# Optimization experiments

Hardware: AMD Instinct MI355X
Metric: run time of the kernel (lower is better)

Reference implementation:

```python
import jax, jax.numpy as jnp
import numpy as np

# ---- social-force / MPDM constants (param object in the original) ----
N = 4096           # number of agents (row 0 = robot)
DT = 0.4           # integration timestep [s]
PED_SPEED = 1.0    # desired pedestrian speed [m/s]
K_ATTR = 2.0       # attractive-force gain k
ALPHA = 10.0       # repulsive-force amplitude
PED_RADIUS = 0.3   # pedestrian radius [m]
PED_MASS = 60.0    # pedestrian mass [kg]
BETTA = 0.71       # repulsion range constant
A_COST = 5.0       # deviation (blame) weight a
B_COST = 2.0       # proximity-blame weight b
E_COST = 1.0       # blame length scale e
EPS = 1e-8


def calc_forces(state, goal):
    pos, vel = state[:, :2], state[:, 2:4]
    # attractive force toward goal: k * (v_desired - v_current)
    to_goal = goal - pos
    dist_g = jnp.sqrt(jnp.sum(to_goal * to_goal, axis=1, keepdims=True) + EPS)
    af = K_ATTR * (PED_SPEED * to_goal / dist_g - vel)
    # pairwise repulsive social force, [N,N,2] interaction tensor
    delta = pos[:, None, :] - pos[None, :, :]                 # [N,N,2]
    dist = jnp.sqrt(jnp.sum(delta * delta, axis=-1) + EPS)    # [N,N]
    mag = ALPHA * jnp.exp((2.0 * PED_RADIUS - dist) / BETTA)  # [N,N]
    mag = mag * (1.0 - jnp.eye(pos.shape[0], dtype=pos.dtype))  # no self-force
    rf = jnp.einsum('ij,ijc->ic', mag / dist, delta) / PED_MASS
    return rf, af


def pose_propagation(F, state):
    pos, vel = state[:, :2], state[:, 2:4]
    new_pos = pos + vel * DT + 0.5 * F * (DT * DT)
    new_vel = vel + F * DT
    spd = jnp.sqrt(jnp.sum(new_vel * new_vel, axis=1, keepdims=True) + EPS)
    new_vel = new_vel * jnp.minimum(1.0, PED_SPEED / spd)  # clamp to max speed
    return jnp.concatenate([new_pos, new_vel], axis=1)


def calc_cost_function(goal, robot_init_pose, out_state, observed_state):
    robot_pose = out_state[0, :2]
    peds = out_state[1:, :2]
    obs = observed_state[1:, :2]
    # progress of robot toward its goal
    pg = (jnp.sqrt(jnp.sum((robot_init_pose - goal[0]) ** 2) + EPS)
          - jnp.sqrt(jnp.sum((robot_pose - goal[0]) ** 2) + EPS))
    # blame: pedestrian deviation from observed trajectory
    deviation = jnp.sum(jnp.sqrt(jnp.sum((peds - obs) ** 2, axis=1) + EPS))
    # blame: robot proximity to pedestrians
    d = jnp.sqrt(jnp.sum((peds - robot_pose) ** 2, axis=1) + EPS)
    blame = jnp.sum(jnp.exp(-d / E_COST))
    return A_COST * deviation + B_COST * blame - pg


def setup_inputs() -> dict:
    key = jax.random.key(0)
    k1, k2, k3, k4 = jax.random.split(key, 4)
    pos = jax.random.normal(k1, (N, 2), dtype=jnp.float32) * 20.0
    vel = jax.random.normal(k2, (N, 2), dtype=jnp.float32)
    state = jnp.concatenate([pos, vel], axis=1)
    goal = jax.random.normal(k3, (N, 2), dtype=jnp.float32) * 20.0
    obs_pos = pos + 0.1 * jax.random.normal(k4, (N, 2), dtype=jnp.float32)
    observed_state = jnp.concatenate([obs_pos, vel], axis=1)
    return {
        'state': state,
        'cost': jnp.zeros((1,), dtype=jnp.float32),
        'stacked_trajectories_for_visualizer': state,
        'goal': goal,
        'observed_state': observed_state,
    }


def reference(state, cost, stacked_trajectories_for_visualizer, goal, observed_state):
    rf, af = calc_forces(state, goal)
    F = rf + af
    output = pose_propagation(F, state)
    temp = calc_cost_function(goal, state[0, :2], output, observed_state)
    new_cost = cost + temp
    stacked = jnp.concatenate([stacked_trajectories_for_visualizer, state], axis=0)
    return (output, new_cost, stacked)
```

## Files before the change

kernel.cpp:

```cpp
#include <hip/hip_runtime.h>

#define NPED 4096
#define SPLIT 32
#define JC (NPED / SPLIT)
#define BI 256
#define EPSF 1e-8f
#define DTF 0.4f
#define INV_MASS (1.0f/60.0f)
#define C1f (-2.0319648463225964f)
#define C0f (4.54110700268092f)
#define NLOG2E (-1.4426950408889634f)

__device__ __forceinline__ float rsqf(float x) { return __builtin_amdgcn_rsqf(x); }
__device__ __forceinline__ float ex2(float x)  { return __builtin_amdgcn_exp2f(x); }

__global__ __launch_bounds__(BI) void forces_kernel(const float4* __restrict__ state,
                                                    float2* __restrict__ part) {
    __shared__ float2 spos[JC];
    const int t  = threadIdx.x;
    const int ib = blockIdx.x;
    const int s  = blockIdx.y;
    if (t < JC) {
        float4 r = state[s * JC + t];
        spos[t] = make_float2(r.x, r.y);
    }
    const int i = ib * BI + t;
    float4 me = state[i];
    __syncthreads();
    const float xi = me.x, yi = me.y;
    float fx = 0.f, fy = 0.f;
    #pragma unroll 8
    for (int j = 0; j < JC; ++j) {
        float2 pj = spos[j];
        float dx = xi - pj.x;
        float dy = yi - pj.y;
        float d2 = fmaf(dx, dx, fmaf(dy, dy, EPSF));
        float inv = rsqf(d2);
        float dist = d2 * inv;
        float w = ex2(fmaf(dist, C1f, C0f)) * inv;
        fx = fmaf(w, dx, fx);
        fy = fmaf(w, dy, fy);
    }
    part[s * NPED + i] = make_float2(fx, fy);
}

__global__ __launch_bounds__(256) void integrate_kernel(const float4* __restrict__ state,
                                                        const float2* __restrict__ goal,
                                                        const float4* __restrict__ stk,
                                                        const float2* __restrict__ part,
                                                        float* __restrict__ out) {
    const int i = blockIdx.x * 256 + threadIdx.x;
    float fx = 0.f, fy = 0.f;
    #pragma unroll
    for (int s = 0; s < SPLIT; ++s) {
        float2 v = part[s * NPED + i];
        fx += v.x; fy += v.y;
    }
    fx *= INV_MASS; fy *= INV_MASS;
    float4 st = state[i];
    float2 g  = goal[i];
    float tx = g.x - st.x, ty = g.y - st.y;
    float invg = rsqf(fmaf(tx, tx, fmaf(ty, ty, EPSF)));
    float Fx = fx + 2.f * fmaf(tx, invg, -st.z);
    float Fy = fy + 2.f * fmaf(ty, invg, -st.w);
    float npx = fmaf(0.08f, Fx, fmaf(DTF, st.z, st.x));
    float npy = fmaf(0.08f, Fy, fmaf(DTF, st.w, st.y));
    float nvx = fmaf(DTF, Fx, st.z);
    float nvy = fmaf(DTF, Fy, st.w);
    float invs = rsqf(fmaf(nvx, nvx, fmaf(nvy, nvy, EPSF)));
    float sc = fminf(1.f, invs);
    nvx *= sc; nvy *= sc;
    ((float4*)out)[i] = make_float4(npx, npy, nvx, nvy);
    float4 sv = stk[i];
    float* o1 = out + (NPED * 4 + 1) + i * 4;
    o1[0] = sv.x; o1[1] = sv.y; o1[2] = sv.z; o1[3] = sv.w;
    float* o2 = o1 + NPED * 4;
    o2[0] = st.x; o2[1] = st.y; o2[2] = st.z; o2[3] = st.w;
}

__global__ __launch_bounds__(1024) void cost_kernel(const float* __restrict__ state,
                                                    const float* __restrict__ cost_in,
                                                    const float* __restrict__ goal,
                                                    const float* __restrict__ obs,
                                                    float* __restrict__ out) {
    const int t = threadIdx.x;
    const float rx = out[0], ry = out[1];
    float dev = 0.f, blame = 0.f;
    for (int i = 1 + t; i < NPED; i += 1024) {
        float px = out[i * 4 + 0], py = out[i * 4 + 1];
        float ox = obs[i * 4 + 0], oy = obs[i * 4 + 1];
        float dxo = px - ox, dyo = py - oy;
        dev += sqrtf(fmaf(dxo, dxo, fmaf(dyo, dyo, EPSF)));
        float dxr = px - rx, dyr = py - ry;
        float d = sqrtf(fmaf(dxr, dxr, fmaf(dyr, dyr, EPSF)));
        blame += ex2(NLOG2E * d);
    }
    #pragma unroll
    for (int off = 32; off > 0; off >>= 1) {
        dev   += __shfl_down(dev, off);
        blame += __shfl_down(blame, off);
    }
    __shared__ float sd[16], sb[16];
    if ((t & 63) == 0) { sd[t >> 6] = dev; sb[t >> 6] = blame; }
    __syncthreads();
    if (t == 0) {
        float D = 0.f, B = 0.f;
        #pragma unroll
        for (int k = 0; k < 16; ++k) { D += sd[k]; B += sb[k]; }
        float gx = goal[0], gy = goal[1];
        float rix = state[0], riy = state[1];
        float a1x = rix - gx, a1y = riy - gy;
        float a2x = rx - gx,  a2y = ry - gy;
        float pg = sqrtf(fmaf(a1x, a1x, fmaf(a1y, a1y, EPSF)))
                 - sqrtf(fmaf(a2x, a2x, fmaf(a2y, a2y, EPSF)));
        out[NPED * 4] = cost_in[0] + 5.f * D + 2.f * B - pg;
    }
}

extern "C" void kernel_launch(void* const* d_in, const int* in_sizes, int n_in,
                              void* d_out, int out_size, void* d_ws, size_t ws_size,
                              hipStream_t stream) {
    const float4* state = (const float4*)d_in[0];
    const float*  cost  = (const float*)d_in[1];
    const float4* stk   = (const float4*)d_in[2];
    const float2* goal  = (const float2*)d_in[3];
    const float*  obs   = (const float*)d_in[4];
    float* out = (float*)d_out;
    float2* part = (float2*)d_ws;

    forces_kernel<<<dim3(NPED / BI, SPLIT), BI, 0, stream>>>(state, part);
    integrate_kernel<<<NPED / 256, 256, 0, stream>>>(state, goal, stk, part, out);
    cost_kernel<<<1, 1024, 0, stream>>>((const float*)state, cost,
                                        (const float*)goal, obs, out);
}
```

Before: 74.15 us.

## Fuse force, integrate and cost kernels into one cooperative kernel with grid syncs

Replaces the three kernel launches with a single cooperative launch of 512 blocks that computes partial forces, does a grid-wide sync, integrates on 16 blocks, syncs again, and reduces the cost on block 0. This removes two launch gaps and inter-kernel dependencies. In exchange it pays for two grid barriers, and the cost reduction now runs on a single 256-thread block instead of a 1024-thread one.

```diff
diff --git a/kernel.cpp b/kernel.cpp
--- a/kernel.cpp
+++ b/kernel.cpp
@@ -1,9 +1,13 @@
 #include <hip/hip_runtime.h>
+#include <hip/hip_cooperative_groups.h>
+
+namespace cg = cooperative_groups;
 
 #define NPED 4096
 #define SPLIT 32
 #define JC (NPED / SPLIT)
 #define BI 256
+#define NBLK (16 * SPLIT)
 #define EPSF 1e-8f
 #define DTF 0.4f
 #define INV_MASS (1.0f/60.0f)
@@ -14,12 +18,20 @@
 __device__ __forceinline__ float rsqf(float x) { return __builtin_amdgcn_rsqf(x); }
 __device__ __forceinline__ float ex2(float x)  { return __builtin_amdgcn_exp2f(x); }
 
-__global__ __launch_bounds__(BI) void forces_kernel(const float4* __restrict__ state,
-                                                    float2* __restrict__ part) {
+__global__ __launch_bounds__(BI) void fused_kernel(const float4* __restrict__ state,
+                                                   const float* __restrict__ cost_in,
+                                                   const float4* __restrict__ stk,
+                                                   const float2* __restrict__ goal,
+                                                   const float* __restrict__ obs,
+                                                   float* __restrict__ out,
+                                                   float2* __restrict__ part) {
+    cg::grid_group grid = cg::this_grid();
+    const int t  = threadIdx.x;
+    const int b  = blockIdx.x;
+    const int ib = b & 15;
+    const int s  = b >> 4;
+
     __shared__ float2 spos[JC];
-    const int t  = threadIdx.x;
-    const int ib = blockIdx.x;
-    const int s  = blockIdx.y;
     if (t < JC) {
         float4 r = state[s * JC + t];
         spos[t] = make_float2(r.x, r.y);
@@ -27,93 +39,92 @@
     const int i = ib * BI + t;
     float4 me = state[i];
     __syncthreads();
-    const float xi = me.x, yi = me.y;
-    float fx = 0.f, fy = 0.f;
-    #pragma unroll 8
-    for (int j = 0; j < JC; ++j) {
-        float2 pj = spos[j];
-        float dx = xi - pj.x;
-        float dy = yi - pj.y;
-        float d2 = fmaf(dx, dx, fmaf(dy, dy, EPSF));
-        float inv = rsqf(d2);
-        float dist = d2 * inv;
-        float w = ex2(fmaf(dist, C1f, C0f)) * inv;
-        fx = fmaf(w, dx, fx);
-        fy = fmaf(w, dy, fy);
+    {
+        const float xi = me.x, yi = me.y;
+        float fx = 0.f, fy = 0.f;
+        #pragma unroll 8
+        for (int j = 0; j < JC; ++j) {
+            float2 pj = spos[j];
+            float dx = xi - pj.x;
+            float dy = yi - pj.y;
+            float d2 = fmaf(dx, dx, fmaf(dy, dy, EPSF));
+            float inv = rsqf(d2);
+            float dist = d2 * inv;
+            float w = ex2(fmaf(dist, C1f, C0f)) * inv;
+            fx = fmaf(w, dx, fx);
+            fy = fmaf(w, dy, fy);
+        }
+        part[s * NPED + i] = make_float2(fx, fy);
     }
-    part[s * NPED + i] = make_float2(fx, fy);
-}
 
-__global__ __launch_bounds__(256) void integrate_kernel(const float4* __restrict__ state,
-                                                        const float2* __restrict__ goal,
-                                                        const float4* __restrict__ stk,
-                                                        const float2* __restrict__ part,
-                                                        float* __restrict__ out) {
-    const int i = blockIdx.x * 256 + threadIdx.x;
-    float fx = 0.f, fy = 0.f;
-    #pragma unroll
-    for (int s = 0; s < SPLIT; ++s) {
-        float2 v = part[s * NPED + i];
-        fx += v.x; fy += v.y;
+    grid.sync();
+
+    if (b < 16) {
+        const int ii = b * BI + t;
+        float fx = 0.f, fy = 0.f;
+        #pragma unroll
+        for (int sp = 0; sp < SPLIT; ++sp) {
+            float2 v = part[sp * NPED + ii];
+            fx += v.x; fy += v.y;
+        }
+        fx *= INV_MASS; fy *= INV_MASS;
+        float4 st = state[ii];
+        float2 g  = goal[ii];
+        float tx = g.x - st.x, ty = g.y - st.y;
+        float invg = rsqf(fmaf(tx, tx, fmaf(ty, ty, EPSF)));
+        float Fx = fx + 2.f * fmaf(tx, invg, -st.z);
+        float Fy = fy + 2.f * fmaf(ty, invg, -st.w);
+        float npx = fmaf(0.08f, Fx, fmaf(DTF, st.z, st.x));
+        float npy = fmaf(0.08f, Fy, fmaf(DTF, st.w, st.y));
+        float nvx = fmaf(DTF, Fx, st.z);
+        float nvy = fmaf(DTF, Fy, st.w);
+        float invs = rsqf(fmaf(nvx, nvx, fmaf(nvy, nvy, EPSF)));
+        float sc = fminf(1.f, invs);
+        nvx *= sc; nvy *= sc;
+        ((float4*)out)[ii] = make_float4(npx, npy, nvx, nvy);
+        float4 sv = stk[ii];
+        float* o1 = out + (NPED * 4 + 1) + ii * 4;
+        o1[0] = sv.x; o1[1] = sv.y; o1[2] = sv.z; o1[3] = sv.w;
+        float* o2 = o1 + NPED * 4;
+        o2[0] = st.x; o2[1] = st.y; o2[2] = st.z; o2[3] = st.w;
     }
-    fx *= INV_MASS; fy *= INV_MASS;
-    float4 st = state[i];
-    float2 g  = goal[i];
-    float tx = g.x - st.x, ty = g.y - st.y;
-    float invg = rsqf(fmaf(tx, tx, fmaf(ty, ty, EPSF)));
-    float Fx = fx + 2.f * fmaf(tx, invg, -st.z);
-    float Fy = fy + 2.f * fmaf(ty, invg, -st.w);
-    float npx = fmaf(0.08f, Fx, fmaf(DTF, st.z, st.x));
-    float npy = fmaf(0.08f, Fy, fmaf(DTF, st.w, st.y));
-    float nvx = fmaf(DTF, Fx, st.z);
-    float nvy = fmaf(DTF, Fy, st.w);
-    float invs = rsqf(fmaf(nvx, nvx, fmaf(nvy, nvy, EPSF)));
-    float sc = fminf(1.f, invs);
-    nvx *= sc; nvy *= sc;
-    ((float4*)out)[i] = make_float4(npx, npy, nvx, nvy);
-    float4 sv = stk[i];
-    float* o1 = out + (NPED * 4 + 1) + i * 4;
-    o1[0] = sv.x; o1[1] = sv.y; o1[2] = sv.z; o1[3] = sv.w;
-    float* o2 = o1 + NPED * 4;
-    o2[0] = st.x; o2[1] = st.y; o2[2] = st.z; o2[3] = st.w;
-}
 
-__global__ __launch_bounds__(1024) void cost_kernel(const float* __restrict__ state,
-                                                    const float* __restrict__ cost_in,
-                                                    const float* __restrict__ goal,
-                                                    const float* __restrict__ obs,
-                                                    float* __restrict__ out) {
-    const int t = threadIdx.x;
-    const float rx = out[0], ry = out[1];
-    float dev = 0.f, blame = 0.f;
-    for (int i = 1 + t; i < NPED; i += 1024) {
-        float px = out[i * 4 + 0], py = out[i * 4 + 1];
-        float ox = obs[i * 4 + 0], oy = obs[i * 4 + 1];
-        float dxo = px - ox, dyo = py - oy;
-        dev += sqrtf(fmaf(dxo, dxo, fmaf(dyo, dyo, EPSF)));
-        float dxr = px - rx, dyr = py - ry;
-        float d = sqrtf(fmaf(dxr, dxr, fmaf(dyr, dyr, EPSF)));
-        blame += ex2(NLOG2E * d);
-    }
-    #pragma unroll
-    for (int off = 32; off > 0; off >>= 1) {
-        dev   += __shfl_down(dev, off);
-        blame += __shfl_down(blame, off);
-    }
-    __shared__ float sd[16], sb[16];
-    if ((t & 63) == 0) { sd[t >> 6] = dev; sb[t >> 6] = blame; }
-    __syncthreads();
-    if (t == 0) {
-        float D = 0.f, B = 0.f;
+    grid.sync();
+
+    if (b == 0) {
+        const float rx = out[0], ry = out[1];
+        float dev = 0.f, blame = 0.f;
+        for (int k = 1 + t; k < NPED; k += BI) {
+            float px = out[k * 4 + 0], py = out[k * 4 + 1];
+            float ox = obs[k * 4 + 0], oy = obs[k * 4 + 1];
+            float dxo = px - ox, dyo = py - oy;
+            dev += sqrtf(fmaf(dxo, dxo, fmaf(dyo, dyo, EPSF)));
+            float dxr = px - rx, dyr = py - ry;
+            float d = sqrtf(fmaf(dxr, dxr, fmaf(dyr, dyr, EPSF)));
+            blame += ex2(NLOG2E * d);
+        }
         #pragma unroll
-        for (int k = 0; k < 16; ++k) { D += sd[k]; B += sb[k]; }
-        float gx = goal[0], gy = goal[1];
-        float rix = state[0], riy = state[1];
-        float a1x = rix - gx, a1y = riy - gy;
-        float a2x = rx - gx,  a2y = ry - gy;
-        float pg = sqrtf(fmaf(a1x, a1x, fmaf(a1y, a1y, EPSF)))
-                 - sqrtf(fmaf(a2x, a2x, fmaf(a2y, a2y, EPSF)));
-        out[NPED * 4] = cost_in[0] + 5.f * D + 2.f * B - pg;
+        for (int off = 32; off > 0; off >>= 1) {
+            dev   += __shfl_down(dev, off);
+            blame += __shfl_down(blame, off);
+        }
+        __shared__ float sd[4], sb[4];
+        if ((t & 63) == 0) { sd[t >> 6] = dev; sb[t >> 6] = blame; }
+        __syncthreads();
+        if (t == 0) {
+            float D = 0.f, B = 0.f;
+            #pragma unroll
+            for (int k = 0; k < 4; ++k) { D += sd[k]; B += sb[k]; }
+            const float* stf = (const float*)state;
+            const float* gf  = (const float*)goal;
+            float gx = gf[0], gy = gf[1];
+            float rix = stf[0], riy = stf[1];
+            float a1x = rix - gx, a1y = riy - gy;
+            float a2x = rx - gx,  a2y = ry - gy;
+            float pg = sqrtf(fmaf(a1x, a1x, fmaf(a1y, a1y, EPSF)))
+                     - sqrtf(fmaf(a2x, a2x, fmaf(a2y, a2y, EPSF)));
+            out[NPED * 4] = cost_in[0] + 5.f * D + 2.f * B - pg;
+        }
     }
 }
 
@@ -125,11 +136,11 @@
     const float4* stk   = (const float4*)d_in[2];
     const float2* goal  = (const float2*)d_in[3];
     const float*  obs   = (const float*)d_in[4];
-    float* out = (float*)d_out;
+    float* out   = (float*)d_out;
     float2* part = (float2*)d_ws;
 
-    forces_kernel<<<dim3(NPED / BI, SPLIT), BI, 0, stream>>>(state, part);
-    integrate_kernel<<<NPED / 256, 256, 0, stream>>>(state, goal, stk, part, out);
-    cost_kernel<<<1, 1024, 0, stream>>>((const float*)state, cost,
-                                        (const float*)goal, obs, out);
+    void* args[] = {(void*)&state, (void*)&cost, (void*)&stk, (void*)&goal,
+                    (void*)&obs, (void*)&out, (void*)&part};
+    hipLaunchCooperativeKernel((void*)fused_kernel, dim3(NBLK), dim3(BI),
+                               args, 0, stream);
 }
```

Result: slower. 180.5 us (+143.4%).
